# Kernel tuning notes

Measured on AMD Instinct MI355X. Metric: run time of the kernel, lower is better.

## Reference

```python
import jax, jax.numpy as jnp
import numpy as np
import math

N_FRAG = 500_000
N_GENES = 5000
N_FREQ = 20
ENC_DIM = N_FREQ * 2 * 2  # 80
EMB_DIM = 5


def setup_inputs() -> dict:
    key = jax.random.key(0)
    k1, k2, k3, k4 = jax.random.split(key, 4)
    coordinates = jax.random.normal(k1, (N_FRAG, 2), dtype=jnp.float32) * 1000.0
    gene_ix = jax.random.randint(k2, (N_FRAG,), 0, N_GENES, dtype=jnp.int64 if jax.config.jax_enable_x64 else jnp.int32)
    # disjoint contiguous groups covering all fragments: 100k groups of 2, 50k of 3, 25k of 4, 10k of 5
    n2 = jnp.arange(0, 200_000, dtype=jnp.int32)
    n3 = jnp.arange(200_000, 350_000, dtype=jnp.int32)
    n4 = jnp.arange(350_000, 450_000, dtype=jnp.int32)
    n5 = jnp.arange(450_000, 500_000, dtype=jnp.int32)
    stdv = 1.0 / math.sqrt(EMB_DIM)
    weight1 = jax.random.uniform(k3, (N_GENES, ENC_DIM, EMB_DIM), dtype=jnp.float32, minval=-stdv, maxval=stdv)
    weight2 = jax.random.uniform(k4, (N_GENES, ENC_DIM, EMB_DIM), dtype=jnp.float32, minval=-stdv, maxval=stdv)
    return {"coordinates": coordinates, "gene_ix": gene_ix, "n2": n2, "n3": n3, "n4": n4, "n5": n5,
            "weight1": weight1, "weight2": weight2}


def _sine_encoding(coordinates):
    # frequencies: each of the N_FREQ frequencies repeated twice; shifts alternate (0, pi/2)
    i = jnp.arange(1, N_FREQ + 1, dtype=coordinates.dtype)
    freqs = jnp.repeat(1.0 / 1000.0 ** (2.0 * i / N_FREQ), 2)            # [2*N_FREQ]
    shifts = jnp.tile(jnp.array([0.0, jnp.pi / 2], coordinates.dtype), N_FREQ)  # [2*N_FREQ]
    # [N, 2, 1] * [2*N_FREQ] -> [N, 2, 2*N_FREQ] -> flatten -> [N, ENC_DIM]
    return jnp.sin(coordinates[..., None] * freqs + shifts).reshape(coordinates.shape[0], -1)


def _group_self_attention(emb, enc_dim_unused, groups):
    # groups: list of (group_size, flat index array); disjoint sets of fragment rows
    D = emb.shape[-1]
    for i, n_ in groups:
        x = emb[n_].reshape(-1, i, D)                                    # [G, i, D]
        scores = jnp.einsum('gid,gjd->gij', x, x) / math.sqrt(i)         # scale by sqrt(group size)
        y = jnp.einsum('gij,gjd->gid', jax.nn.softmax(scores, axis=-1), x)
        emb = emb.at[n_].set(y.reshape(-1, D))
    return emb


def reference(coordinates, gene_ix, n2, n3, n4, n5, weight1, weight2):
    enc = _sine_encoding(coordinates)                                    # [N, 80]
    # per-fragment gather of gene weight matrix, contract over encoding dim
    emb = jax.nn.sigmoid(jnp.einsum('ne,ned->nd', enc, weight1[gene_ix]))  # [N, 5]
    # NOTE: original forward computes embedding_att from weight2 but never uses it (dead code)
    emb = _group_self_attention(emb, enc, [(2, n2), (3, n3), (4, n4), (5, n5)])
    return emb
```

## Files before the change

kernel.cpp:

```cpp
#include <hip/hip_runtime.h>
#include <hip/hip_bf16.h>
#include <math.h>

#define N_FRAG 500000
#define N_GENES 5000
#define EMB_DIM 5
#define NFREQ 20
#define CAP 256
#define SCAT_BLOCKS ((N_FRAG + 255) / 256)
#define ATTN_BLOCKS 723

static constexpr float FREQS[20] = {
    5.011872336272722e-01f, 2.511886431509580e-01f, 1.258925411794167e-01f,
    6.309573444801933e-02f, 3.162277660168379e-02f, 1.584893192461113e-02f,
    7.943282347242814e-03f, 3.981071705534973e-03f, 1.995262314968880e-03f,
    1.000000000000000e-03f, 5.011872336272725e-04f, 2.511886431509580e-04f,
    1.258925411794167e-04f, 6.309573444801934e-05f, 3.162277660168379e-05f,
    1.584893192461114e-05f, 7.943282347242822e-06f, 3.981071705534973e-06f,
    1.995262314968879e-06f, 1.000000000000000e-06f
};
#define INV2PI 0.15915494309189535f

__global__ void __launch_bounds__(256) scatter_cap_kernel(
    const int* __restrict__ gene_ix, const float* __restrict__ coords,
    int* __restrict__ cursor, float2* __restrict__ cg2, int* __restrict__ sortedN)
{
    int i = blockIdx.x * blockDim.x + threadIdx.x;
    if (i >= N_FRAG) return;
    int g = gene_ix[i];
    int pos = atomicAdd(&cursor[g], 1);
    if (pos < CAP) {
        float2 c = reinterpret_cast<const float2*>(coords)[i];
        cg2[(size_t)g * CAP + pos] = c;
        sortedN[(size_t)g * CAP + pos] = i;
    }
}

__global__ void __launch_bounds__(256) emb_gene_kernel(
    const int* __restrict__ cursor, const int* __restrict__ sortedN,
    const float2* __restrict__ cg2, const float* __restrict__ w1,
    float* __restrict__ out)
{
    __shared__ float wlds[400];
    const int g   = blockIdx.x;
    const int tid = threadIdx.x;

    const float4* __restrict__ Wg4 =
        reinterpret_cast<const float4*>(w1 + (size_t)g * 400);
    if (tid < 100)
        reinterpret_cast<float4*>(wlds)[tid] = Wg4[tid];

    int cnt = min(cursor[g], CAP);
    __syncthreads();

    if (tid >= cnt) return;

    int n = sortedN[(size_t)g * CAP + tid];
    float2 c = cg2[(size_t)g * CAP + tid];
    float cx = c.x, cy = c.y;

    const float* __restrict__ W = wlds;
    float a0 = 0.f, a1 = 0.f, a2 = 0.f, a3 = 0.f, a4 = 0.f;
#pragma unroll
    for (int k = 0; k < NFREQ; ++k) {
        const float gf = FREQS[k] * INV2PI;
        float rx = cx * gf; rx -= floorf(rx);
        float ry = cy * gf; ry -= floorf(ry);
        float s0 = __builtin_amdgcn_sinf(rx);
        float c0 = __builtin_amdgcn_cosf(rx);
        float s1 = __builtin_amdgcn_sinf(ry);
        float c1 = __builtin_amdgcn_cosf(ry);

        const float* p0 = W + 10 * k;
        const float* p1 = W + 200 + 10 * k;
        a0 = fmaf(s0, p0[0], fmaf(c0, p0[5], fmaf(s1, p1[0], fmaf(c1, p1[5], a0))));
        a1 = fmaf(s0, p0[1], fmaf(c0, p0[6], fmaf(s1, p1[1], fmaf(c1, p1[6], a1))));
        a2 = fmaf(s0, p0[2], fmaf(c0, p0[7], fmaf(s1, p1[2], fmaf(c1, p1[7], a2))));
        a3 = fmaf(s0, p0[3], fmaf(c0, p0[8], fmaf(s1, p1[3], fmaf(c1, p1[8], a3))));
        a4 = fmaf(s0, p0[4], fmaf(c0, p0[9], fmaf(s1, p1[4], fmaf(c1, p1[9], a4))));
    }

    float* o = out + (size_t)n * EMB_DIM;
    o[0] = 1.f / (1.f + __expf(-a0));
    o[1] = 1.f / (1.f + __expf(-a1));
    o[2] = 1.f / (1.f + __expf(-a2));
    o[3] = 1.f / (1.f + __expf(-a3));
    o[4] = 1.f / (1.f + __expf(-a4));
}

template <int S>
__device__ __forceinline__ void attn_one_inplace(float* __restrict__ p) {
    float x[S][EMB_DIM];
#pragma unroll
    for (int i = 0; i < S; ++i)
#pragma unroll
        for (int d = 0; d < EMB_DIM; ++d) x[i][d] = p[i * EMB_DIM + d];
    const float inv_scale = 1.f / sqrtf((float)S);
    float y[S][EMB_DIM];
#pragma unroll
    for (int i = 0; i < S; ++i) {
        float sc[S]; float m = -1e30f;
#pragma unroll
        for (int j = 0; j < S; ++j) {
            float s = 0.f;
#pragma unroll
            for (int d = 0; d < EMB_DIM; ++d) s = fmaf(x[i][d], x[j][d], s);
            sc[j] = s * inv_scale; m = fmaxf(m, sc[j]);
        }
        float sum = 0.f;
#pragma unroll
        for (int j = 0; j < S; ++j) { sc[j] = __expf(sc[j] - m); sum += sc[j]; }
        float r = 1.f / sum;
#pragma unroll
        for (int d = 0; d < EMB_DIM; ++d) {
            float a = 0.f;
#pragma unroll
            for (int j = 0; j < S; ++j) a = fmaf(sc[j], x[j][d], a);
            y[i][d] = a * r;
        }
    }
#pragma unroll
    for (int i = 0; i < S; ++i)
#pragma unroll
        for (int d = 0; d < EMB_DIM; ++d) p[i * EMB_DIM + d] = y[i][d];
}

__global__ void __launch_bounds__(256) attn_inplace_kernel(float* __restrict__ out) {
    int t = blockIdx.x * blockDim.x + threadIdx.x;
    if (t < 100000)      attn_one_inplace<2>(out + (size_t)(2 * t) * EMB_DIM);
    else if (t < 150000) attn_one_inplace<3>(out + (size_t)(200000 + 3 * (t - 100000)) * EMB_DIM);
    else if (t < 175000) attn_one_inplace<4>(out + (size_t)(350000 + 4 * (t - 150000)) * EMB_DIM);
    else if (t < 185000) attn_one_inplace<5>(out + (size_t)(450000 + 5 * (t - 175000)) * EMB_DIM);
}

__global__ void __launch_bounds__(256) emb_direct_kernel(
    const float* __restrict__ coords,
    const int* __restrict__ gene_ix,
    const float* __restrict__ weight1,
    float* __restrict__ out)
{
    int n = blockIdx.x * blockDim.x + threadIdx.x;
    if (n >= N_FRAG) return;
    float cx = coords[2 * n], cy = coords[2 * n + 1];
    float enc[80];
#pragma unroll
    for (int i = 0; i < NFREQ; ++i) {
        const float g = FREQS[i] * INV2PI;
        float rx = cx * g; rx -= floorf(rx);
        float ry = cy * g; ry -= floorf(ry);
        enc[2 * i]          = __builtin_amdgcn_sinf(rx);
        enc[2 * i + 1]      = __builtin_amdgcn_cosf(rx);
        enc[40 + 2 * i]     = __builtin_amdgcn_sinf(ry);
        enc[40 + 2 * i + 1] = __builtin_amdgcn_cosf(ry);
    }
    const float4* __restrict__ W4 =
        reinterpret_cast<const float4*>(weight1 + (size_t)gene_ix[n] * 400);
    float acc[EMB_DIM] = {0.f, 0.f, 0.f, 0.f, 0.f};
#pragma unroll
    for (int j = 0; j < 100; ++j) {
        float4 w = W4[j];
        const int k0 = 4 * j;
        acc[(k0 + 0) % 5] = fmaf(enc[(k0 + 0) / 5], w.x, acc[(k0 + 0) % 5]);
        acc[(k0 + 1) % 5] = fmaf(enc[(k0 + 1) / 5], w.y, acc[(k0 + 1) % 5]);
        acc[(k0 + 2) % 5] = fmaf(enc[(k0 + 2) / 5], w.z, acc[(k0 + 2) % 5]);
        acc[(k0 + 3) % 5] = fmaf(enc[(k0 + 3) / 5], w.w, acc[(k0 + 3) % 5]);
    }
    float* o = out + (size_t)n * EMB_DIM;
#pragma unroll
    for (int d = 0; d < EMB_DIM; ++d)
        o[d] = 1.f / (1.f + __expf(-acc[d]));
}

extern "C" void kernel_launch(void* const* d_in, const int* in_sizes, int n_in,
                              void* d_out, int out_size, void* d_ws, size_t ws_size,
                              hipStream_t stream) {
    const float* coords  = (const float*)d_in[0];
    const int*   gene_ix = (const int*)d_in[1];
    const float* weight1 = (const float*)d_in[6];
    float* out = (float*)d_out;

    const size_t off_cursor  = 0;
    const size_t off_cg2     = 0x10000;
    const size_t off_sortedN = 0x9D8000;
    const size_t need        = off_sortedN + (size_t)N_GENES * CAP * 4;

    if (ws_size >= need) {
        int*    cursor  = (int*)((char*)d_ws + off_cursor);
        float2* cg2     = (float2*)((char*)d_ws + off_cg2);
        int*    sortedN = (int*)((char*)d_ws + off_sortedN);

        hipMemsetAsync(cursor, 0, N_GENES * sizeof(int), stream);
        scatter_cap_kernel<<<SCAT_BLOCKS, 256, 0, stream>>>(
            gene_ix, coords, cursor, cg2, sortedN);
        emb_gene_kernel<<<N_GENES, 256, 0, stream>>>(
            cursor, sortedN, cg2, weight1, out);
        attn_inplace_kernel<<<ATTN_BLOCKS, 256, 0, stream>>>(out);
    } else {
        const int nb_frag = (N_FRAG + 255) / 256;
        emb_direct_kernel<<<nb_frag, 256, 0, stream>>>(coords, gene_ix, weight1, out);
        attn_inplace_kernel<<<ATTN_BLOCKS, 256, 0, stream>>>(out);
    }
}
```

Measured before the change: 70.85 us.

## Partition gene bucket cursors per XCD to localize scatter atomics

Splits each gene's bucket into 8 sub-sections keyed by blockIdx&7, which on MI355X matches the round-robin assignment of blocks to XCDs. Each section gets its own padded atomic counter, so atomics from different dies no longer contend on the same cache line and stay local to one die's L2. The gene kernel now walks 512 slots in two passes and checks per-section counts. The cost is a larger workspace and memset, and 2x more sparse slot reads. A section overflowing 64 entries would drop fragments, but with about 100 fragments per gene spread over 8 sections that is unlikely.

```diff
diff --git a/kernel.cpp b/kernel.cpp
--- a/kernel.cpp
+++ b/kernel.cpp
@@ -6,7 +6,11 @@
 #define N_GENES 5000
 #define EMB_DIM 5
 #define NFREQ 20
-#define CAP 256
+#define NR 8
+#define SECCAP 64
+#define GCAP (NR * SECCAP)
+#define CURSTRIDE 4
+#define CURN 5120
 #define SCAT_BLOCKS ((N_FRAG + 255) / 256)
 #define ATTN_BLOCKS 723
 
@@ -21,18 +25,19 @@
 };
 #define INV2PI 0.15915494309189535f
 
-__global__ void __launch_bounds__(256) scatter_cap_kernel(
+__global__ void __launch_bounds__(256) scatter_xcd_kernel(
     const int* __restrict__ gene_ix, const float* __restrict__ coords,
     int* __restrict__ cursor, float2* __restrict__ cg2, int* __restrict__ sortedN)
 {
+    const int r = blockIdx.x & (NR - 1);
     int i = blockIdx.x * blockDim.x + threadIdx.x;
     if (i >= N_FRAG) return;
     int g = gene_ix[i];
-    int pos = atomicAdd(&cursor[g], 1);
-    if (pos < CAP) {
-        float2 c = reinterpret_cast<const float2*>(coords)[i];
-        cg2[(size_t)g * CAP + pos] = c;
-        sortedN[(size_t)g * CAP + pos] = i;
+    int pos = atomicAdd(&cursor[((size_t)r * CURN + g) * CURSTRIDE], 1);
+    if (pos < SECCAP) {
+        size_t slot = (size_t)g * GCAP + r * SECCAP + pos;
+        cg2[slot] = reinterpret_cast<const float2*>(coords)[i];
+        sortedN[slot] = i;
     }
 }
 
@@ -42,6 +47,7 @@
     float* __restrict__ out)
 {
     __shared__ float wlds[400];
+    __shared__ int cnts[NR];
     const int g   = blockIdx.x;
     const int tid = threadIdx.x;
 
@@ -49,43 +55,50 @@
         reinterpret_cast<const float4*>(w1 + (size_t)g * 400);
     if (tid < 100)
         reinterpret_cast<float4*>(wlds)[tid] = Wg4[tid];
-
-    int cnt = min(cursor[g], CAP);
+    if (tid < NR)
+        cnts[tid] = min(cursor[((size_t)tid * CURN + g) * CURSTRIDE], SECCAP);
     __syncthreads();
 
-    if (tid >= cnt) return;
-
-    int n = sortedN[(size_t)g * CAP + tid];
-    float2 c = cg2[(size_t)g * CAP + tid];
-    float cx = c.x, cy = c.y;
-
     const float* __restrict__ W = wlds;
-    float a0 = 0.f, a1 = 0.f, a2 = 0.f, a3 = 0.f, a4 = 0.f;
-#pragma unroll
-    for (int k = 0; k < NFREQ; ++k) {
-        const float gf = FREQS[k] * INV2PI;
-        float rx = cx * gf; rx -= floorf(rx);
-        float ry = cy * gf; ry -= floorf(ry);
-        float s0 = __builtin_amdgcn_sinf(rx);
-        float c0 = __builtin_amdgcn_cosf(rx);
-        float s1 = __builtin_amdgcn_sinf(ry);
-        float c1 = __builtin_amdgcn_cosf(ry);
-
-        const float* p0 = W + 10 * k;
-        const float* p1 = W + 200 + 10 * k;
-        a0 = fmaf(s0, p0[0], fmaf(c0, p0[5], fmaf(s1, p1[0], fmaf(c1, p1[5], a0))));
-        a1 = fmaf(s0, p0[1], fmaf(c0, p0[6], fmaf(s1, p1[1], fmaf(c1, p1[6], a1))));
-        a2 = fmaf(s0, p0[2], fmaf(c0, p0[7], fmaf(s1, p1[2], fmaf(c1, p1[7], a2))));
-        a3 = fmaf(s0, p0[3], fmaf(c0, p0[8], fmaf(s1, p1[3], fmaf(c1, p1[8], a3))));
-        a4 = fmaf(s0, p0[4], fmaf(c0, p0[9], fmaf(s1, p1[4], fmaf(c1, p1[9], a4))));
-    }
-
-    float* o = out + (size_t)n * EMB_DIM;
-    o[0] = 1.f / (1.f + __expf(-a0));
-    o[1] = 1.f / (1.f + __expf(-a1));
-    o[2] = 1.f / (1.f + __expf(-a2));
-    o[3] = 1.f / (1.f + __expf(-a3));
-    o[4] = 1.f / (1.f + __expf(-a4));
+#pragma unroll
+    for (int pass = 0; pass < 2; ++pass) {
+        int s = tid + pass * 256;
+        int r = s >> 6;
+        int idx = s & (SECCAP - 1);
+        if (idx >= cnts[r]) continue;
+
+        size_t slot = (size_t)g * GCAP + s;
+        int n = sortedN[slot];
+        float2 c = cg2[slot];
+        float cx = c.x, cy = c.y;
+
+        float a0 = 0.f, a1 = 0.f, a2 = 0.f, a3 = 0.f, a4 = 0.f;
+#pragma unroll
+        for (int k = 0; k < NFREQ; ++k) {
+            const float gf = FREQS[k] * INV2PI;
+            float rx = cx * gf; rx -= floorf(rx);
+            float ry = cy * gf; ry -= floorf(ry);
+            float s0 = __builtin_amdgcn_sinf(rx);
+            float c0 = __builtin_amdgcn_cosf(rx);
+            float s1 = __builtin_amdgcn_sinf(ry);
+            float c1 = __builtin_amdgcn_cosf(ry);
+
+            const float* p0 = W + 10 * k;
+            const float* p1 = W + 200 + 10 * k;
+            a0 = fmaf(s0, p0[0], fmaf(c0, p0[5], fmaf(s1, p1[0], fmaf(c1, p1[5], a0))));
+            a1 = fmaf(s0, p0[1], fmaf(c0, p0[6], fmaf(s1, p1[1], fmaf(c1, p1[6], a1))));
+            a2 = fmaf(s0, p0[2], fmaf(c0, p0[7], fmaf(s1, p1[2], fmaf(c1, p1[7], a2))));
+            a3 = fmaf(s0, p0[3], fmaf(c0, p0[8], fmaf(s1, p1[3], fmaf(c1, p1[8], a3))));
+            a4 = fmaf(s0, p0[4], fmaf(c0, p0[9], fmaf(s1, p1[4], fmaf(c1, p1[9], a4))));
+        }
+
+        float* o = out + (size_t)n * EMB_DIM;
+        o[0] = 1.f / (1.f + __expf(-a0));
+        o[1] = 1.f / (1.f + __expf(-a1));
+        o[2] = 1.f / (1.f + __expf(-a2));
+        o[3] = 1.f / (1.f + __expf(-a3));
+        o[4] = 1.f / (1.f + __expf(-a4));
+    }
 }
 
 template <int S>
@@ -179,18 +192,19 @@
     const float* weight1 = (const float*)d_in[6];
     float* out = (float*)d_out;
 
-    const size_t off_cursor  = 0;
-    const size_t off_cg2     = 0x10000;
-    const size_t off_sortedN = 0x9D8000;
-    const size_t need        = off_sortedN + (size_t)N_GENES * CAP * 4;
+    const size_t cursor_bytes = (size_t)NR * CURN * CURSTRIDE * 4;
+    const size_t off_cursor   = 0;
+    const size_t off_cg2      = 0xA0000;
+    const size_t off_sortedN  = 0x1430000;
+    const size_t need         = off_sortedN + (size_t)N_GENES * GCAP * 4;
 
     if (ws_size >= need) {
         int*    cursor  = (int*)((char*)d_ws + off_cursor);
         float2* cg2     = (float2*)((char*)d_ws + off_cg2);
         int*    sortedN = (int*)((char*)d_ws + off_sortedN);
 
-        hipMemsetAsync(cursor, 0, N_GENES * sizeof(int), stream);
-        scatter_cap_kernel<<<SCAT_BLOCKS, 256, 0, stream>>>(
+        hipMemsetAsync(cursor, 0, cursor_bytes, stream);
+        scatter_xcd_kernel<<<SCAT_BLOCKS, 256, 0, stream>>>(
             gene_ix, coords, cursor, cg2, sortedN);
         emb_gene_kernel<<<N_GENES, 256, 0, stream>>>(
             cursor, sortedN, cg2, weight1, out);
```

Result: slower. 88.63 us (+25.1%).
